# Kernel tuning notes

Hardware: AMD Instinct MI355X
Metric: run time of the kernel (lower is better)

## Reference

```python
import jax, jax.numpy as jnp
import numpy as np

N_NODES = 100000
IN_CH, HIDDEN, OUT_CH = 128, 128, 64
N_POS, N_NEG = 600000, 600000


def _glorot(key, shape):
    lim = float(np.sqrt(6.0 / (shape[0] + shape[1])))
    return jax.random.uniform(key, shape, jnp.float32, -lim, lim)


def setup_inputs() -> dict:
    key = jax.random.key(0)
    k = jax.random.split(key, 7)
    x = jax.random.normal(k[0], (N_NODES, IN_CH), jnp.float32)
    pos_edge_index = jax.random.randint(k[1], (2, N_POS), 0, N_NODES, jnp.int64)
    neg_edge_index = jax.random.randint(k[2], (2, N_NEG), 0, N_NODES, jnp.int64)
    W1 = _glorot(k[3], (IN_CH, HIDDEN))
    b1 = jnp.zeros((HIDDEN,), jnp.float32)
    W2 = _glorot(k[4], (HIDDEN, OUT_CH))
    b2 = jnp.zeros((OUT_CH,), jnp.float32)
    return {"x": x, "pos_edge_index": pos_edge_index, "neg_edge_index": neg_edge_index,
            "W1": W1, "b1": b1, "W2": W2, "b2": b2}


def gcn_conv(x, W, b, src, dst, n_nodes):
    # PyG GCNConv: add self-loops, symmetric deg^-1/2 normalization, linear, bias
    h = x @ W                                               # [N, F_out]
    ones = jnp.ones(src.shape, h.dtype)
    deg = jax.ops.segment_sum(ones, dst, num_segments=n_nodes) + 1.0  # self-loop
    dinv = jax.lax.rsqrt(deg)                               # deg^-0.5, deg >= 1
    norm = dinv[src] * dinv[dst]                            # per-edge norm
    agg = jax.ops.segment_sum(h[src] * norm[:, None], dst, num_segments=n_nodes)
    agg = agg + h * (dinv * dinv)[:, None]                  # self-loop messages
    return agg + b


def reference(x, pos_edge_index, neg_edge_index, W1, b1, W2, b2):
    n = x.shape[0]
    src, dst = pos_edge_index[0], pos_edge_index[1]
    z = gcn_conv(x, W1, b1, src, dst, n)
    z = jax.nn.relu(z)
    z = gcn_conv(z, W2, b2, src, dst, n)
    # decode: gather endpoints of pos+neg edges, elementwise product, sum over feat
    ei = jnp.concatenate([pos_edge_index, neg_edge_index], axis=-1)  # [2, E_pos+E_neg]
    return jnp.sum(z[ei[0]] * z[ei[1]], axis=-1)
```

## Files before the change

kernel.cpp:

```cpp
#include <hip/hip_runtime.h>

#define N_NODES 100000
#define IN_CH 128
#define HIDDEN 128
#define OUT_CH 64
#define N_POS 600000
#define N_NEG 600000

typedef unsigned int uint32;
typedef unsigned short ushort16;
typedef __attribute__((ext_vector_type(8))) short bf16x8;
typedef __attribute__((ext_vector_type(4))) float f32x4;

__device__ inline float bf_lo(uint32 u) {
    union { uint32 i; float f; } v;
    v.i = u << 16;
    return v.f;
}
__device__ inline float bf_hi(uint32 u) {
    union { uint32 i; float f; } v;
    v.i = u & 0xffff0000u;
    return v.f;
}
__device__ inline ushort16 f2bf(float f) {
    union { uint32 i; float f; } v;
    v.f = f;
    uint32 r = v.i + 0x7fffu + ((v.i >> 16) & 1u);
    return (ushort16)(r >> 16);
}
__device__ inline uint32 pack2bf(float a, float b) {
    return (uint32)f2bf(a) | ((uint32)f2bf(b) << 16);
}

__global__ void hist_count(const int* __restrict__ dst, int* __restrict__ hist, int n_edges) {
    int i = blockIdx.x * blockDim.x + threadIdx.x;
    if (i < n_edges) atomicAdd(&hist[dst[i]], 1);
}

__global__ void scan_reduce(const int* __restrict__ hist, int* __restrict__ partials, int n) {
    __shared__ int sdata[256];
    int b = blockIdx.x, t = threadIdx.x;
    int base = b * 1024;
    int s = 0;
    for (int i = t; i < 1024; i += 256) {
        int idx = base + i;
        s += (idx < n) ? hist[idx] : 0;
    }
    sdata[t] = s;
    __syncthreads();
    for (int off = 128; off > 0; off >>= 1) {
        if (t < off) sdata[t] += sdata[t + off];
        __syncthreads();
    }
    if (t == 0) partials[b] = sdata[0];
}

__global__ void scan_partials(int* __restrict__ partials, int nb) {
    __shared__ int tmp[128];
    int t = threadIdx.x;
    int v = (t < nb) ? partials[t] : 0;
    tmp[t] = v;
    __syncthreads();
    for (int off = 1; off < 128; off <<= 1) {
        int a = (t >= off) ? tmp[t - off] : 0;
        __syncthreads();
        tmp[t] += a;
        __syncthreads();
    }
    if (t < nb) partials[t] = tmp[t] - v;
}

__global__ void scan_final(const int* __restrict__ hist, const int* __restrict__ partials,
                           int* __restrict__ rowstart, int* __restrict__ cursor,
                           float* __restrict__ dinv, int n) {
    __shared__ int tsum[256];
    int t = threadIdx.x, b = blockIdx.x;
    int base = b * 1024 + t * 4;
    int v[4];
    int s = 0;
#pragma unroll
    for (int j = 0; j < 4; j++) {
        int i = base + j;
        v[j] = (i < n) ? hist[i] : 0;
        s += v[j];
    }
    tsum[t] = s;
    __syncthreads();
    for (int off = 1; off < 256; off <<= 1) {
        int a = (t >= off) ? tsum[t - off] : 0;
        __syncthreads();
        tsum[t] += a;
        __syncthreads();
    }
    int offset = partials[b] + (tsum[t] - s);
#pragma unroll
    for (int j = 0; j < 4; j++) {
        int i = base + j;
        if (i < n) {
            rowstart[i] = offset;
            cursor[i] = offset;
            dinv[i] = rsqrtf((float)v[j] + 1.0f);
            offset += v[j];
        }
    }
    if (b == 0 && t == 0) rowstart[n] = N_POS;
}

__global__ void csr_fill(const int* __restrict__ src, const int* __restrict__ dst,
                         const float* __restrict__ dinv, int* __restrict__ cursor,
                         int* __restrict__ adj, float* __restrict__ wgt, int n_edges) {
    int e = blockIdx.x * blockDim.x + threadIdx.x;
    if (e < n_edges) {
        int s = src[e], d = dst[e];
        int p = atomicAdd(&cursor[d], 1);
        adj[p] = s;
        wgt[p] = dinv[s] * dinv[d];
    }
}

__global__ void wt_convert(const float* __restrict__ W1, const float* __restrict__ W2,
                           ushort16* __restrict__ W1t, ushort16* __restrict__ W2t) {
    int i = blockIdx.x * blockDim.x + threadIdx.x;
    if (i < 128 * 128) {
        int n = i >> 7, k = i & 127;
        W1t[i] = f2bf(W1[k * 128 + n]);
    } else {
        int j = i - 128 * 128;
        if (j < 64 * 128) {
            int n = j >> 7, k = j & 127;
            W2t[j] = f2bf(W2[k * 64 + n]);
        }
    }
}

template <int M, bool XBF>
__global__ __launch_bounds__(256) void gemm_mfma(const void* __restrict__ Xv,
                                                const ushort16* __restrict__ Wt,
                                                ushort16* __restrict__ H, int n) {
    constexpr int K = 128;
    constexpr int TN = 64;
    constexpr int XS = 136;
    __shared__ short Xs[TN * XS];
    __shared__ short Ws[M * XS];
    int tid = threadIdx.x;
    int node0 = blockIdx.x * TN;

    for (int q = tid; q < M * K / 8; q += 256) {
        int row = q >> 4;
        int c = q & 15;
        uint4 v = ((const uint4*)Wt)[q];
        *(uint4*)(Ws + row * XS + c * 8) = v;
    }
    if (!XBF) {
        const float* X = (const float*)Xv;
        int row = tid >> 2, part = tid & 3;
        int gn = node0 + row;
#pragma unroll
        for (int c = 0; c < 8; ++c) {
            int k = part * 32 + c * 4;
            float4 v = (gn < n) ? *(const float4*)(X + (size_t)gn * K + k) : float4{0, 0, 0, 0};
            uint2 p = {pack2bf(v.x, v.y), pack2bf(v.z, v.w)};
            *(uint2*)(Xs + row * XS + k) = p;
        }
    } else {
        const ushort16* X = (const ushort16*)Xv;
        for (int q = tid; q < TN * K / 8; q += 256) {
            int row = q >> 4;
            int c = q & 15;
            int gn = node0 + row;
            uint4 v = (gn < n) ? ((const uint4*)(X + (size_t)gn * K))[c] : uint4{0, 0, 0, 0};
            *(uint4*)(Xs + row * XS + c * 8) = v;
        }
    }
    __syncthreads();

    constexpr int CT = M / 16;
    int w = tid >> 6;
    int lane = tid & 63;
    int l15 = lane & 15;
    int quad = lane >> 4;

    f32x4 acc[CT] = {};
    const short* xrow = Xs + (w * 16 + l15) * XS + quad * 8;
#pragma unroll
    for (int kk = 0; kk < 4; ++kk) {
        bf16x8 a = *(const bf16x8*)(xrow + kk * 32);
#pragma unroll
        for (int ct = 0; ct < CT; ++ct) {
            bf16x8 b = *(const bf16x8*)(Ws + (ct * 16 + l15) * XS + quad * 8 + kk * 32);
            acc[ct] = __builtin_amdgcn_mfma_f32_16x16x32_bf16(a, b, acc[ct], 0, 0, 0);
        }
    }

#pragma unroll
    for (int ct = 0; ct < CT; ++ct) {
#pragma unroll
        for (int r = 0; r < 4; ++r) {
            int gn = node0 + w * 16 + quad * 4 + r;
            if (gn < n) H[(size_t)gn * M + ct * 16 + l15] = f2bf(acc[ct][r]);
        }
    }
}

template <int F, bool RELU>
__global__ void agg_pull(const int* __restrict__ rowstart, const int* __restrict__ adj,
                         const float* __restrict__ wgt, const float* __restrict__ dinv,
                         const ushort16* __restrict__ H, const float* __restrict__ bias,
                         ushort16* __restrict__ Z, int n) {
    int g = threadIdx.x >> 5;
    int l = threadIdx.x & 31;
    int node = blockIdx.x * (blockDim.x >> 5) + g;
    if (node >= n) return;
    float dn = dinv[node];
    int rs = rowstart[node], re = rowstart[node + 1];
    if (F == 128) {
        float ac[4][4] = {};
        int p = rs;
        for (; p + 4 <= re; p += 4) {
            int s0 = adj[p], s1 = adj[p + 1], s2 = adj[p + 2], s3 = adj[p + 3];
            float w0 = wgt[p], w1 = wgt[p + 1], w2 = wgt[p + 2], w3 = wgt[p + 3];
            uint2 h0 = *(const uint2*)(H + (size_t)s0 * F + l * 4);
            uint2 h1 = *(const uint2*)(H + (size_t)s1 * F + l * 4);
            uint2 h2 = *(const uint2*)(H + (size_t)s2 * F + l * 4);
            uint2 h3 = *(const uint2*)(H + (size_t)s3 * F + l * 4);
            ac[0][0] += bf_lo(h0.x) * w0; ac[0][1] += bf_hi(h0.x) * w0;
            ac[0][2] += bf_lo(h0.y) * w0; ac[0][3] += bf_hi(h0.y) * w0;
            ac[1][0] += bf_lo(h1.x) * w1; ac[1][1] += bf_hi(h1.x) * w1;
            ac[1][2] += bf_lo(h1.y) * w1; ac[1][3] += bf_hi(h1.y) * w1;
            ac[2][0] += bf_lo(h2.x) * w2; ac[2][1] += bf_hi(h2.x) * w2;
            ac[2][2] += bf_lo(h2.y) * w2; ac[2][3] += bf_hi(h2.y) * w2;
            ac[3][0] += bf_lo(h3.x) * w3; ac[3][1] += bf_hi(h3.x) * w3;
            ac[3][2] += bf_lo(h3.y) * w3; ac[3][3] += bf_hi(h3.y) * w3;
        }
        for (; p < re; ++p) {
            int s = adj[p];
            float w = wgt[p];
            uint2 h = *(const uint2*)(H + (size_t)s * F + l * 4);
            ac[0][0] += bf_lo(h.x) * w; ac[0][1] += bf_hi(h.x) * w;
            ac[0][2] += bf_lo(h.y) * w; ac[0][3] += bf_hi(h.y) * w;
        }
        uint2 hv = *(const uint2*)(H + (size_t)node * F + l * 4);
        float4 bv = *(const float4*)(bias + l * 4);
        float d2 = dn * dn;
        float v0 = (ac[0][0] + ac[1][0]) + (ac[2][0] + ac[3][0]) + bf_lo(hv.x) * d2 + bv.x;
        float v1 = (ac[0][1] + ac[1][1]) + (ac[2][1] + ac[3][1]) + bf_hi(hv.x) * d2 + bv.y;
        float v2 = (ac[0][2] + ac[1][2]) + (ac[2][2] + ac[3][2]) + bf_lo(hv.y) * d2 + bv.z;
        float v3 = (ac[0][3] + ac[1][3]) + (ac[2][3] + ac[3][3]) + bf_hi(hv.y) * d2 + bv.w;
        if (RELU) {
            v0 = fmaxf(v0, 0.0f); v1 = fmaxf(v1, 0.0f);
            v2 = fmaxf(v2, 0.0f); v3 = fmaxf(v3, 0.0f);
        }
        *(uint2*)(Z + (size_t)node * F + l * 4) = uint2{pack2bf(v0, v1), pack2bf(v2, v3)};
    } else {
        float ax0 = 0, ay0 = 0, ax1 = 0, ay1 = 0, ax2 = 0, ay2 = 0, ax3 = 0, ay3 = 0;
        int p = rs;
        for (; p + 4 <= re; p += 4) {
            int s0 = adj[p], s1 = adj[p + 1], s2 = adj[p + 2], s3 = adj[p + 3];
            float w0 = wgt[p], w1 = wgt[p + 1], w2 = wgt[p + 2], w3 = wgt[p + 3];
            uint32 h0 = *(const uint32*)(H + (size_t)s0 * F + l * 2);
            uint32 h1 = *(const uint32*)(H + (size_t)s1 * F + l * 2);
            uint32 h2 = *(const uint32*)(H + (size_t)s2 * F + l * 2);
            uint32 h3 = *(const uint32*)(H + (size_t)s3 * F + l * 2);
            ax0 += bf_lo(h0) * w0; ay0 += bf_hi(h0) * w0;
            ax1 += bf_lo(h1) * w1; ay1 += bf_hi(h1) * w1;
            ax2 += bf_lo(h2) * w2; ay2 += bf_hi(h2) * w2;
            ax3 += bf_lo(h3) * w3; ay3 += bf_hi(h3) * w3;
        }
        for (; p < re; ++p) {
            int s = adj[p];
            float w = wgt[p];
            uint32 h = *(const uint32*)(H + (size_t)s * F + l * 2);
            ax0 += bf_lo(h) * w;
            ay0 += bf_hi(h) * w;
        }
        float ax = (ax0 + ax1) + (ax2 + ax3);
        float ay = (ay0 + ay1) + (ay2 + ay3);
        uint32 hv = *(const uint32*)(H + (size_t)node * F + l * 2);
        float2 bv = *(const float2*)(bias + l * 2);
        float d2 = dn * dn;
        float vx = ax + bf_lo(hv) * d2 + bv.x;
        float vy = ay + bf_hi(hv) * d2 + bv.y;
        if (RELU) {
            vx = fmaxf(vx, 0.0f);
            vy = fmaxf(vy, 0.0f);
        }
        *(uint32*)(Z + (size_t)node * F + l * 2) = pack2bf(vx, vy);
    }
}

__global__ void decode_mfma(const int* __restrict__ pos, const int* __restrict__ neg,
                            const short* __restrict__ Z, float* __restrict__ out) {
    int wid = threadIdx.x >> 6;
    int lane = threadIdx.x & 63;
    int l15 = lane & 15;
    int quad = lane >> 4;
    int e0 = (blockIdx.x * 4 + wid) * 16;
    if (e0 >= N_POS + N_NEG) return;
    const int* bp = (e0 < N_POS) ? pos : (neg - N_POS);
    int e = e0 + l15;
    int a = bp[e];
    int b = bp[600000 + e];

    const short* za = Z + (size_t)a * OUT_CH + quad * 8;
    const short* zb = Z + (size_t)b * OUT_CH + quad * 8;
    bf16x8 a0 = *(const bf16x8*)(za);
    bf16x8 a1 = *(const bf16x8*)(za + 32);
    bf16x8 b0 = *(const bf16x8*)(zb);
    bf16x8 b1 = *(const bf16x8*)(zb + 32);

    f32x4 acc = {};
    acc = __builtin_amdgcn_mfma_f32_16x16x32_bf16(a0, b0, acc, 0, 0, 0);
    acc = __builtin_amdgcn_mfma_f32_16x16x32_bf16(a1, b1, acc, 0, 0, 0);

    if (quad == (l15 >> 2)) out[e] = acc[l15 & 3];
}

extern "C" void kernel_launch(void* const* d_in, const int* in_sizes, int n_in,
                              void* d_out, int out_size, void* d_ws, size_t ws_size,
                              hipStream_t stream) {
    const float* x = (const float*)d_in[0];
    const int* pos = (const int*)d_in[1];
    const int* neg = (const int*)d_in[2];
    const float* W1 = (const float*)d_in[3];
    const float* b1 = (const float*)d_in[4];
    const float* W2 = (const float*)d_in[5];
    const float* b2 = (const float*)d_in[6];
    float* out = (float*)d_out;

    ushort16* A = (ushort16*)d_ws;
    ushort16* B = A + (size_t)N_NODES * 128;
    float* dinv = (float*)(B + (size_t)N_NODES * 128);
    int* hist = (int*)(dinv + N_NODES);
    int* rowstart = hist + N_NODES;
    int* cursor = rowstart + N_NODES + 1;
    int* adj = cursor + N_NODES;
    float* wgt = (float*)(adj + N_POS);
    int* partials = (int*)(wgt + N_POS);
    ushort16* W1t = (ushort16*)(partials + 128);
    ushort16* W2t = W1t + 128 * 128;

    const int* pos_src = pos;
    const int* pos_dst = pos + N_POS;

    constexpr int NB_SCAN = (N_NODES + 1023) / 1024;

    hipMemsetAsync(hist, 0, N_NODES * sizeof(int), stream);
    hist_count<<<(N_POS + 255) / 256, 256, 0, stream>>>(pos_dst, hist, N_POS);
    scan_reduce<<<NB_SCAN, 256, 0, stream>>>(hist, partials, N_NODES);
    scan_partials<<<1, 128, 0, stream>>>(partials, NB_SCAN);
    scan_final<<<NB_SCAN, 256, 0, stream>>>(hist, partials, rowstart, cursor, dinv, N_NODES);
    csr_fill<<<(N_POS + 255) / 256, 256, 0, stream>>>(pos_src, pos_dst, dinv, cursor, adj, wgt,
                                                      N_POS);
    wt_convert<<<(128 * 128 + 64 * 128 + 255) / 256, 256, 0, stream>>>(W1, W2, W1t, W2t);

    gemm_mfma<HIDDEN, false><<<(N_NODES + 63) / 64, 256, 0, stream>>>(x, W1t, A, N_NODES);
    agg_pull<HIDDEN, true><<<(N_NODES + 7) / 8, 256, 0, stream>>>(rowstart, adj, wgt, dinv, A, b1,
                                                                  B, N_NODES);

    ushort16* h2 = A;
    gemm_mfma<OUT_CH, true><<<(N_NODES + 63) / 64, 256, 0, stream>>>(B, W2t, h2, N_NODES);
    ushort16* z2 = B;
    agg_pull<OUT_CH, false><<<(N_NODES + 7) / 8, 256, 0, stream>>>(rowstart, adj, wgt, dinv, h2,
                                                                   b2, z2, N_NODES);

    decode_mfma<<<(N_POS + N_NEG) / 64, 256, 0, stream>>>(pos, neg, (const short*)z2, out);
}
```

Before: 304.0 us.

## Interleave CSR neighbor index and weight; use 16 lanes per node in aggregation

Stores each CSR entry's source index and normalization weight together as one int2, so the aggregation kernels do one 8-byte load per edge instead of two separate 4-byte loads from different arrays. Aggregation now assigns 16 lanes per node instead of 32. Each lane loads 16 bytes per neighbor for F=128 and 8 bytes for F=64, so each wave covers twice as many nodes and issues fewer, wider gather loads. The trade-off is more accumulator registers per thread and longer per-lane loops, which may lower occupancy.

```diff
diff --git a/kernel.cpp b/kernel.cpp
--- a/kernel.cpp
+++ b/kernel.cpp
@@ -108,13 +108,12 @@
 
 __global__ void csr_fill(const int* __restrict__ src, const int* __restrict__ dst,
                          const float* __restrict__ dinv, int* __restrict__ cursor,
-                         int* __restrict__ adj, float* __restrict__ wgt, int n_edges) {
+                         int2* __restrict__ adjw, int n_edges) {
     int e = blockIdx.x * blockDim.x + threadIdx.x;
     if (e < n_edges) {
         int s = src[e], d = dst[e];
         int p = atomicAdd(&cursor[d], 1);
-        adj[p] = s;
-        wgt[p] = dinv[s] * dinv[d];
+        adjw[p] = int2{s, __float_as_int(dinv[s] * dinv[d])};
     }
 }
 
@@ -203,26 +202,79 @@
 }
 
 template <int F, bool RELU>
-__global__ void agg_pull(const int* __restrict__ rowstart, const int* __restrict__ adj,
-                         const float* __restrict__ wgt, const float* __restrict__ dinv,
-                         const ushort16* __restrict__ H, const float* __restrict__ bias,
-                         ushort16* __restrict__ Z, int n) {
-    int g = threadIdx.x >> 5;
-    int l = threadIdx.x & 31;
-    int node = blockIdx.x * (blockDim.x >> 5) + g;
+__global__ void agg_pull(const int* __restrict__ rowstart, const int2* __restrict__ adjw,
+                         const float* __restrict__ dinv, const ushort16* __restrict__ H,
+                         const float* __restrict__ bias, ushort16* __restrict__ Z, int n) {
+    int g = threadIdx.x >> 4;
+    int l = threadIdx.x & 15;
+    int node = blockIdx.x * (blockDim.x >> 4) + g;
     if (node >= n) return;
     float dn = dinv[node];
     int rs = rowstart[node], re = rowstart[node + 1];
     if (F == 128) {
+        float ac[4][8] = {};
+        int p = rs;
+        for (; p + 4 <= re; p += 4) {
+            int2 e0 = adjw[p], e1 = adjw[p + 1], e2 = adjw[p + 2], e3 = adjw[p + 3];
+            uint4 h0 = *(const uint4*)(H + (size_t)e0.x * F + l * 8);
+            uint4 h1 = *(const uint4*)(H + (size_t)e1.x * F + l * 8);
+            uint4 h2 = *(const uint4*)(H + (size_t)e2.x * F + l * 8);
+            uint4 h3 = *(const uint4*)(H + (size_t)e3.x * F + l * 8);
+            float w0 = __int_as_float(e0.y), w1 = __int_as_float(e1.y);
+            float w2 = __int_as_float(e2.y), w3 = __int_as_float(e3.y);
+            ac[0][0] += bf_lo(h0.x) * w0; ac[0][1] += bf_hi(h0.x) * w0;
+            ac[0][2] += bf_lo(h0.y) * w0; ac[0][3] += bf_hi(h0.y) * w0;
+            ac[0][4] += bf_lo(h0.z) * w0; ac[0][5] += bf_hi(h0.z) * w0;
+            ac[0][6] += bf_lo(h0.w) * w0; ac[0][7] += bf_hi(h0.w) * w0;
+            ac[1][0] += bf_lo(h1.x) * w1; ac[1][1] += bf_hi(h1.x) * w1;
+            ac[1][2] += bf_lo(h1.y) * w1; ac[1][3] += bf_hi(h1.y) * w1;
+            ac[1][4] += bf_lo(h1.z) * w1; ac[1][5] += bf_hi(h1.z) * w1;
+            ac[1][6] += bf_lo(h1.w) * w1; ac[1][7] += bf_hi(h1.w) * w1;
+            ac[2][0] += bf_lo(h2.x) * w2; ac[2][1] += bf_hi(h2.x) * w2;
+            ac[2][2] += bf_lo(h2.y) * w2; ac[2][3] += bf_hi(h2.y) * w2;
+            ac[2][4] += bf_lo(h2.z) * w2; ac[2][5] += bf_hi(h2.z) * w2;
+            ac[2][6] += bf_lo(h2.w) * w2; ac[2][7] += bf_hi(h2.w) * w2;
+            ac[3][0] += bf_lo(h3.x) * w3; ac[3][1] += bf_hi(h3.x) * w3;
+            ac[3][2] += bf_lo(h3.y) * w3; ac[3][3] += bf_hi(h3.y) * w3;
+            ac[3][4] += bf_lo(h3.z) * w3; ac[3][5] += bf_hi(h3.z) * w3;
+            ac[3][6] += bf_lo(h3.w) * w3; ac[3][7] += bf_hi(h3.w) * w3;
+        }
+        for (; p < re; ++p) {
+            int2 e = adjw[p];
+            float w = __int_as_float(e.y);
+            uint4 h = *(const uint4*)(H + (size_t)e.x * F + l * 8);
+            ac[0][0] += bf_lo(h.x) * w; ac[0][1] += bf_hi(h.x) * w;
+            ac[0][2] += bf_lo(h.y) * w; ac[0][3] += bf_hi(h.y) * w;
+            ac[0][4] += bf_lo(h.z) * w; ac[0][5] += bf_hi(h.z) * w;
+            ac[0][6] += bf_lo(h.w) * w; ac[0][7] += bf_hi(h.w) * w;
+        }
+        uint4 hv = *(const uint4*)(H + (size_t)node * F + l * 8);
+        float4 bv0 = *(const float4*)(bias + l * 8);
+        float4 bv1 = *(const float4*)(bias + l * 8 + 4);
+        float d2 = dn * dn;
+        float v[8];
+        float hs[8] = {bf_lo(hv.x), bf_hi(hv.x), bf_lo(hv.y), bf_hi(hv.y),
+                       bf_lo(hv.z), bf_hi(hv.z), bf_lo(hv.w), bf_hi(hv.w)};
+        float bb[8] = {bv0.x, bv0.y, bv0.z, bv0.w, bv1.x, bv1.y, bv1.z, bv1.w};
+#pragma unroll
+        for (int j = 0; j < 8; ++j) {
+            v[j] = (ac[0][j] + ac[1][j]) + (ac[2][j] + ac[3][j]) + hs[j] * d2 + bb[j];
+            if (RELU) v[j] = fmaxf(v[j], 0.0f);
+        }
+        *(uint4*)(Z + (size_t)node * F + l * 8) =
+            uint4{pack2bf(v[0], v[1]), pack2bf(v[2], v[3]), pack2bf(v[4], v[5]),
+                  pack2bf(v[6], v[7])};
+    } else {
         float ac[4][4] = {};
         int p = rs;
         for (; p + 4 <= re; p += 4) {
-            int s0 = adj[p], s1 = adj[p + 1], s2 = adj[p + 2], s3 = adj[p + 3];
-            float w0 = wgt[p], w1 = wgt[p + 1], w2 = wgt[p + 2], w3 = wgt[p + 3];
-            uint2 h0 = *(const uint2*)(H + (size_t)s0 * F + l * 4);
-            uint2 h1 = *(const uint2*)(H + (size_t)s1 * F + l * 4);
-            uint2 h2 = *(const uint2*)(H + (size_t)s2 * F + l * 4);
-            uint2 h3 = *(const uint2*)(H + (size_t)s3 * F + l * 4);
+            int2 e0 = adjw[p], e1 = adjw[p + 1], e2 = adjw[p + 2], e3 = adjw[p + 3];
+            uint2 h0 = *(const uint2*)(H + (size_t)e0.x * F + l * 4);
+            uint2 h1 = *(const uint2*)(H + (size_t)e1.x * F + l * 4);
+            uint2 h2 = *(const uint2*)(H + (size_t)e2.x * F + l * 4);
+            uint2 h3 = *(const uint2*)(H + (size_t)e3.x * F + l * 4);
+            float w0 = __int_as_float(e0.y), w1 = __int_as_float(e1.y);
+            float w2 = __int_as_float(e2.y), w3 = __int_as_float(e3.y);
             ac[0][0] += bf_lo(h0.x) * w0; ac[0][1] += bf_hi(h0.x) * w0;
             ac[0][2] += bf_lo(h0.y) * w0; ac[0][3] += bf_hi(h0.y) * w0;
             ac[1][0] += bf_lo(h1.x) * w1; ac[1][1] += bf_hi(h1.x) * w1;
@@ -233,58 +285,24 @@
             ac[3][2] += bf_lo(h3.y) * w3; ac[3][3] += bf_hi(h3.y) * w3;
         }
         for (; p < re; ++p) {
-            int s = adj[p];
-            float w = wgt[p];
-            uint2 h = *(const uint2*)(H + (size_t)s * F + l * 4);
+            int2 e = adjw[p];
+            float w = __int_as_float(e.y);
+            uint2 h = *(const uint2*)(H + (size_t)e.x * F + l * 4);
             ac[0][0] += bf_lo(h.x) * w; ac[0][1] += bf_hi(h.x) * w;
             ac[0][2] += bf_lo(h.y) * w; ac[0][3] += bf_hi(h.y) * w;
         }
         uint2 hv = *(const uint2*)(H + (size_t)node * F + l * 4);
         float4 bv = *(const float4*)(bias + l * 4);
         float d2 = dn * dn;
-        float v0 = (ac[0][0] + ac[1][0]) + (ac[2][0] + ac[3][0]) + bf_lo(hv.x) * d2 + bv.x;
-        float v1 = (ac[0][1] + ac[1][1]) + (ac[2][1] + ac[3][1]) + bf_hi(hv.x) * d2 + bv.y;
-        float v2 = (ac[0][2] + ac[1][2]) + (ac[2][2] + ac[3][2]) + bf_lo(hv.y) * d2 + bv.z;
-        float v3 = (ac[0][3] + ac[1][3]) + (ac[2][3] + ac[3][3]) + bf_hi(hv.y) * d2 + bv.w;
-        if (RELU) {
-            v0 = fmaxf(v0, 0.0f); v1 = fmaxf(v1, 0.0f);
-            v2 = fmaxf(v2, 0.0f); v3 = fmaxf(v3, 0.0f);
-        }
-        *(uint2*)(Z + (size_t)node * F + l * 4) = uint2{pack2bf(v0, v1), pack2bf(v2, v3)};
-    } else {
-        float ax0 = 0, ay0 = 0, ax1 = 0, ay1 = 0, ax2 = 0, ay2 = 0, ax3 = 0, ay3 = 0;
-        int p = rs;
-        for (; p + 4 <= re; p += 4) {
-            int s0 = adj[p], s1 = adj[p + 1], s2 = adj[p + 2], s3 = adj[p + 3];
-            float w0 = wgt[p], w1 = wgt[p + 1], w2 = wgt[p + 2], w3 = wgt[p + 3];
-            uint32 h0 = *(const uint32*)(H + (size_t)s0 * F + l * 2);
-            uint32 h1 = *(const uint32*)(H + (size_t)s1 * F + l * 2);
-            uint32 h2 = *(const uint32*)(H + (size_t)s2 * F + l * 2);
-            uint32 h3 = *(const uint32*)(H + (size_t)s3 * F + l * 2);
-            ax0 += bf_lo(h0) * w0; ay0 += bf_hi(h0) * w0;
-            ax1 += bf_lo(h1) * w1; ay1 += bf_hi(h1) * w1;
-            ax2 += bf_lo(h2) * w2; ay2 += bf_hi(h2) * w2;
-            ax3 += bf_lo(h3) * w3; ay3 += bf_hi(h3) * w3;
-        }
-        for (; p < re; ++p) {
-            int s = adj[p];
-            float w = wgt[p];
-            uint32 h = *(const uint32*)(H + (size_t)s * F + l * 2);
-            ax0 += bf_lo(h) * w;
-            ay0 += bf_hi(h) * w;
-        }
-        float ax = (ax0 + ax1) + (ax2 + ax3);
-        float ay = (ay0 + ay1) + (ay2 + ay3);
-        uint32 hv = *(const uint32*)(H + (size_t)node * F + l * 2);
-        float2 bv = *(const float2*)(bias + l * 2);
-        float d2 = dn * dn;
-        float vx = ax + bf_lo(hv) * d2 + bv.x;
-        float vy = ay + bf_hi(hv) * d2 + bv.y;
-        if (RELU) {
-            vx = fmaxf(vx, 0.0f);
-            vy = fmaxf(vy, 0.0f);
-        }
-        *(uint32*)(Z + (size_t)node * F + l * 2) = pack2bf(vx, vy);
+        float hs[4] = {bf_lo(hv.x), bf_hi(hv.x), bf_lo(hv.y), bf_hi(hv.y)};
+        float bb[4] = {bv.x, bv.y, bv.z, bv.w};
+        float v[4];
+#pragma unroll
+        for (int j = 0; j < 4; ++j) {
+            v[j] = (ac[0][j] + ac[1][j]) + (ac[2][j] + ac[3][j]) + hs[j] * d2 + bb[j];
+            if (RELU) v[j] = fmaxf(v[j], 0.0f);
+        }
+        *(uint2*)(Z + (size_t)node * F + l * 4) = uint2{pack2bf(v[0], v[1]), pack2bf(v[2], v[3])};
     }
 }
 
@@ -333,9 +351,8 @@
     int* hist = (int*)(dinv + N_NODES);
     int* rowstart = hist + N_NODES;
     int* cursor = rowstart + N_NODES + 1;
-    int* adj = cursor + N_NODES;
-    float* wgt = (float*)(adj + N_POS);
-    int* partials = (int*)(wgt + N_POS);
+    int2* adjw = (int2*)(cursor + N_NODES);
+    int* partials = (int*)(adjw + N_POS);
     ushort16* W1t = (ushort16*)(partials + 128);
     ushort16* W2t = W1t + 128 * 128;
 
@@ -349,19 +366,19 @@
     scan_reduce<<<NB_SCAN, 256, 0, stream>>>(hist, partials, N_NODES);
     scan_partials<<<1, 128, 0, stream>>>(partials, NB_SCAN);
     scan_final<<<NB_SCAN, 256, 0, stream>>>(hist, partials, rowstart, cursor, dinv, N_NODES);
-    csr_fill<<<(N_POS + 255) / 256, 256, 0, stream>>>(pos_src, pos_dst, dinv, cursor, adj, wgt,
+    csr_fill<<<(N_POS + 255) / 256, 256, 0, stream>>>(pos_src, pos_dst, dinv, cursor, adjw,
                                                       N_POS);
     wt_convert<<<(128 * 128 + 64 * 128 + 255) / 256, 256, 0, stream>>>(W1, W2, W1t, W2t);
 
     gemm_mfma<HIDDEN, false><<<(N_NODES + 63) / 64, 256, 0, stream>>>(x, W1t, A, N_NODES);
-    agg_pull<HIDDEN, true><<<(N_NODES + 7) / 8, 256, 0, stream>>>(rowstart, adj, wgt, dinv, A, b1,
-                                                                  B, N_NODES);
+    agg_pull<HIDDEN, true><<<(N_NODES + 15) / 16, 256, 0, stream>>>(rowstart, adjw, dinv, A, b1,
+                                                                    B, N_NODES);
 
     ushort16* h2 = A;
     gemm_mfma<OUT_CH, true><<<(N_NODES + 63) / 64, 256, 0, stream>>>(B, W2t, h2, N_NODES);
     ushort16* z2 = B;
-    agg_pull<OUT_CH, false><<<(N_NODES + 7) / 8, 256, 0, stream>>>(rowstart, adj, wgt, dinv, h2,
-                                                                   b2, z2, N_NODES);
+    agg_pull<OUT_CH, false><<<(N_NODES + 15) / 16, 256, 0, stream>>>(rowstart, adjw, dinv, h2, b2,
+                                                                     z2, N_NODES);
 
     decode_mfma<<<(N_POS + N_NEG) / 64, 256, 0, stream>>>(pos, neg, (const short*)z2, out);
 }
```

Result: faster. 289.6 us (-4.7%).
